# Kernel optimization log

Measured on AMD Instinct MI355X. Metric: run time of the kernel, lower is better.

The kernel has to match this reference:

```python
import jax, jax.numpy as jnp
import numpy as np

N_NODES = 30000
N_EDGES = 480000
N_REL = 16
DIM = 128
N_TRIPLES = 200000


def _xavier(key, shape):
    fan_in, fan_out = shape[-2], shape[-1]
    limit = np.sqrt(6.0 / (fan_in + fan_out)).astype(np.float32)
    return jax.random.uniform(key, shape, jnp.float32, -limit, limit)


def setup_inputs() -> dict:
    key = jax.random.key(0)
    ks = jax.random.split(key, 12)
    inp = {
        "node_emb": _xavier(ks[0], (N_NODES, DIM)),
        "rel_emb": _xavier(ks[1], (N_REL, DIM)),
        "W_rel0": _xavier(ks[2], (N_REL, DIM, DIM)),
        "Wself_w0": _xavier(ks[3], (DIM, DIM)),
        "Wself_b0": jnp.zeros((DIM,), jnp.float32),
        "W_rel1": _xavier(ks[4], (N_REL, DIM, DIM)),
        "Wself_w1": _xavier(ks[5], (DIM, DIM)),
        "Wself_b1": jnp.zeros((DIM,), jnp.float32),
        "local_nodes": jnp.arange(N_NODES, dtype=jnp.int32),
        "edge_index": jax.random.randint(ks[6], (2, N_EDGES), 0, N_NODES, jnp.int32),
        "edge_type": jax.random.randint(ks[7], (N_EDGES,), 0, N_REL, jnp.int32),
        "h_loc": jax.random.randint(ks[8], (N_TRIPLES,), 0, N_NODES, jnp.int32),
        "r_ids": jax.random.randint(ks[9], (N_TRIPLES,), 0, N_REL, jnp.int32),
        "t_loc": jax.random.randint(ks[10], (N_TRIPLES,), 0, N_NODES, jnp.int32),
    }
    return inp


def _rgcn_layer(x, edge_index, edge_type, W_rel, Ww, Wb):
    # x: [N, in], W_rel: [R, in, out], Ww: [out, in] (torch Linear layout)
    N = x.shape[0]
    out = x @ Ww.T + Wb                                 # self loop [N, out]
    src, dst = edge_index[0], edge_index[1]
    # transform every node under every relation, then gather per edge:
    # math-equivalent to bmm(x[src][:,None,:], W_rel[rel]) in the original,
    # but avoids materializing [E, in, out].
    xt = jnp.einsum('ni,rio->rno', x, W_rel)            # [R, N, out]
    msg = xt[edge_type, src]                            # [E, out]
    agg = jax.ops.segment_sum(msg, dst, num_segments=N)  # [N, out]
    deg = jax.ops.segment_sum(jnp.ones(dst.shape, x.dtype), dst, num_segments=N)
    deg = jnp.maximum(deg, 1.0)[:, None]
    return jax.nn.relu(out + agg / deg)


def reference(node_emb, rel_emb, W_rel0, Wself_w0, Wself_b0,
              W_rel1, Wself_w1, Wself_b1,
              local_nodes, edge_index, edge_type, h_loc, r_ids, t_loc):
    x = node_emb[local_nodes]                           # [N, d]
    x = _rgcn_layer(x, edge_index, edge_type, W_rel0, Wself_w0, Wself_b0)
    x = _rgcn_layer(x, edge_index, edge_type, W_rel1, Wself_w1, Wself_b1)
    # DistMult scoring on local embeddings
    scores = jnp.sum(x[h_loc] * rel_emb[r_ids] * x[t_loc], axis=-1)  # [B]
    return scores
```

## Files before the change

### kernel.cpp

```cpp
#include <hip/hip_runtime.h>

#define NN 30000
#define NE 480000
#define NR 16
#define D  128
#define NT 200000
#define AST 132
#define NBLK 235
#define NBINS (NBLK * NR)
#define PF 16


__global__ void k_gather_x(const float* __restrict__ node_emb,
                           const int* __restrict__ local_nodes,
                           float* __restrict__ x) {
  int i4 = blockIdx.x * blockDim.x + threadIdx.x;
  if (i4 >= NN * (D / 4)) return;
  int n = i4 >> 5, c = i4 & 31;
  int src = local_nodes[n];
  reinterpret_cast<float4*>(x)[i4] =
      reinterpret_cast<const float4*>(node_emb)[(size_t)src * 32 + c];
}

__global__ void k_hist_bins(const int* __restrict__ ei, const int* __restrict__ et,
                            int* __restrict__ bins) {
  int e = blockIdx.x * blockDim.x + threadIdx.x;
  if (e >= NE) return;
  int d = ei[NE + e], r = et[e];
  atomicAdd(&bins[(d >> 7) * NR + r], 1);
}

__global__ void k_scan_bins(const int* __restrict__ bins, int* __restrict__ off,
                            int* __restrict__ cur) {
  __shared__ int ps[1024];
  const int t = threadIdx.x;
  const int base = t * 4;
  int c[4], s0 = 0;
#pragma unroll
  for (int u = 0; u < 4; ++u) {
    int b = base + u;
    c[u] = (b < NBINS) ? bins[b] : 0;
    s0 += c[u];
  }
  ps[t] = s0;
  __syncthreads();
  for (int dstep = 1; dstep < 1024; dstep <<= 1) {
    int v = (t >= dstep) ? ps[t - dstep] : 0;
    __syncthreads();
    ps[t] += v;
    __syncthreads();
  }
  int ex = ps[t] - s0;
#pragma unroll
  for (int u = 0; u < 4; ++u) {
    int b = base + u;
    if (b <= NBINS) {
      off[b] = ex;
      if (b < NBINS) cur[b] = ex;
    }
    ex += c[u];
  }
}

__global__ void k_fill(const int* __restrict__ ei, const int* __restrict__ et,
                       int* __restrict__ cur, int* __restrict__ srt,
                       float* __restrict__ deg) {
  int e = blockIdx.x * blockDim.x + threadIdx.x;
  if (e >= NE) return;
  int s = ei[e], d = ei[NE + e], r = et[e];
  int p = atomicAdd(&cur[(d >> 7) * NR + r], 1);
  srt[p] = ((d & 127) << 16) | s;
  atomicAdd(&deg[d], 1.0f);
}

__global__ void k_transposeW(const float* __restrict__ W0, const float* __restrict__ W1,
                             float* __restrict__ T0, float* __restrict__ T1) {
  const float* W = blockIdx.x ? W1 : W0;
  float* T = blockIdx.x ? T1 : T0;
  for (int idx = threadIdx.x; idx < D * D; idx += 256) {
    int o = idx >> 7, k = idx & 127;
    T[k * D + o] = W[idx];
  }
}


__device__ __forceinline__ void gemm_tile(const float (*S)[AST],
                                          const float* __restrict__ Wg,
                                          int tx, int ty, float acc[8][4]) {
  const float4* __restrict__ W4 = reinterpret_cast<const float4*>(Wg);
#pragma unroll 8
  for (int k = 0; k < D; k += 4) {
    float4 a[8];
#pragma unroll
    for (int j = 0; j < 8; ++j)
      a[j] = *reinterpret_cast<const float4*>(&S[ty + 16 * j][k]);
    float4 w[4];
#pragma unroll
    for (int kk = 0; kk < 4; ++kk) w[kk] = W4[(k + kk) * 32 + tx];
#pragma unroll
    for (int kk = 0; kk < 4; ++kk) {
#pragma unroll
      for (int j = 0; j < 8; ++j) {
        float av = (kk == 0) ? a[j].x : (kk == 1) ? a[j].y
                 : (kk == 2) ? a[j].z : a[j].w;
        acc[j][0] += av * w[kk].x;
        acc[j][1] += av * w[kk].y;
        acc[j][2] += av * w[kk].z;
        acc[j][3] += av * w[kk].w;
      }
    }
  }
}

__launch_bounds__(512, 2)
__global__ void k_fused(const float* __restrict__ x, const float* __restrict__ Wrel,
                        const float* __restrict__ WT, const float* __restrict__ Wb,
                        const int* __restrict__ srt, const int* __restrict__ off,
                        const float* __restrict__ deg, float* __restrict__ xo) {
  __shared__ float S[D][AST];
  const int nb = blockIdx.x;
  const int row0 = nb * D;
  const int tx = threadIdx.x & 31, ty = threadIdx.x >> 5;
  const int wave = threadIdx.x >> 6, lane = threadIdx.x & 63;
  const float2* __restrict__ x2 = reinterpret_cast<const float2*>(x);

  float acc[8][4];
#pragma unroll
  for (int j = 0; j < 8; ++j)
#pragma unroll
    for (int m = 0; m < 4; ++m) acc[j][m] = 0.f;

  int pv[PF];
  float2 pvv[PF];

  auto zeroS = [&]() {
    float4* S4 = reinterpret_cast<float4*>(&S[0][0]);
#pragma unroll
    for (int t = 0; t < 9; ++t) {
      int idx = threadIdx.x + 512 * t;
      if (idx < D * AST / 4) S4[idx] = make_float4(0.f, 0.f, 0.f, 0.f);
    }
  };
  auto loadE = [&](int b) {
    const int base = off[b], end = off[b + 1];
#pragma unroll
    for (int t = 0; t < PF; ++t) {
      int i = base + wave + 8 * t;
      pv[t] = (i < end) ? srt[i] : -1;
    }
#pragma unroll
    for (int t = 0; t < PF; ++t)
      pvv[t] = (pv[t] >= 0) ? x2[(size_t)(pv[t] & 0xFFFF) * 64 + lane]
                            : make_float2(0.f, 0.f);
  };
  auto depositE = [&](int b) {
#pragma unroll
    for (int t = 0; t < PF; ++t)
      if (pv[t] >= 0) {
        int dl = pv[t] >> 16;
        atomicAdd(&S[dl][2 * lane], pvv[t].x);
        atomicAdd(&S[dl][2 * lane + 1], pvv[t].y);
      }
    const int end = off[b + 1];
    for (int i = off[b] + 8 * PF + wave; i < end; i += 8) {
      int p = srt[i];
      float2 vv = x2[(size_t)(p & 0xFFFF) * 64 + lane];
      atomicAdd(&S[p >> 16][2 * lane], vv.x);
      atomicAdd(&S[p >> 16][2 * lane + 1], vv.y);
    }
  };

  zeroS();
  __syncthreads();
  loadE(nb * NR);
  depositE(nb * NR);

  for (int r = 0; r < NR; ++r) {
    __syncthreads();
    if (r + 1 < NR) loadE(nb * NR + r + 1);
    gemm_tile(S, Wrel + (size_t)r * D * D, tx, ty, acc);
    __syncthreads();
    zeroS();
    __syncthreads();
    if (r + 1 < NR) depositE(nb * NR + r + 1);
  }

#pragma unroll
  for (int j = 0; j < 8; ++j) {
    int row = row0 + ty + 16 * j;
    float dv = (row < NN) ? deg[row] : 1.f;
    float inv = 1.f / fmaxf(dv, 1.f);
#pragma unroll
    for (int m = 0; m < 4; ++m) acc[j][m] *= inv;
  }

#pragma unroll
  for (int t = 0; t < 8; ++t) {
    int idx = threadIdx.x + 512 * t;
    int rw = idx >> 5, c = idx & 31;
    float4 vv = make_float4(0.f, 0.f, 0.f, 0.f);
    if (row0 + rw < NN)
      vv = reinterpret_cast<const float4*>(x)[(size_t)(row0 + rw) * 32 + c];
    *reinterpret_cast<float4*>(&S[rw][4 * c]) = vv;
  }
  __syncthreads();
  gemm_tile(S, WT, tx, ty, acc);

  const float4 bb = reinterpret_cast<const float4*>(Wb)[tx];
#pragma unroll
  for (int j = 0; j < 8; ++j) {
    int row = row0 + ty + 16 * j;
    if (row < NN) {
      float4 o;
      o.x = fmaxf(acc[j][0] + bb.x, 0.f);
      o.y = fmaxf(acc[j][1] + bb.y, 0.f);
      o.z = fmaxf(acc[j][2] + bb.z, 0.f);
      o.w = fmaxf(acc[j][3] + bb.w, 0.f);
      reinterpret_cast<float4*>(xo + (size_t)row * D)[tx] = o;
    }
  }
}


__global__ void k_score(const float* __restrict__ x, const float* __restrict__ rel,
                        const int* __restrict__ hh, const int* __restrict__ rr,
                        const int* __restrict__ tt, float* __restrict__ out) {
  int gw = (blockIdx.x * blockDim.x + threadIdx.x) >> 6;
  int lane = threadIdx.x & 63;
  int nw = (gridDim.x * blockDim.x) >> 6;
  for (int i = gw; i < NT; i += nw) {
    const float2* ph = reinterpret_cast<const float2*>(x + (size_t)hh[i] * D);
    const float2* pr = reinterpret_cast<const float2*>(rel + (size_t)rr[i] * D);
    const float2* pt = reinterpret_cast<const float2*>(x + (size_t)tt[i] * D);
    float2 a = ph[lane], b = pr[lane], c = pt[lane];
    float v = a.x * b.x * c.x + a.y * b.y * c.y;
#pragma unroll
    for (int m = 32; m; m >>= 1) v += __shfl_xor(v, m);
    if (lane == 0) out[i] = v;
  }
}


extern "C" void kernel_launch(void* const* d_in, const int* in_sizes, int n_in,
                              void* d_out, int out_size, void* d_ws, size_t ws_size,
                              hipStream_t stream) {
  const float* node_emb = (const float*)d_in[0];
  const float* rel_emb  = (const float*)d_in[1];
  const float* W_rel0   = (const float*)d_in[2];
  const float* Wself_w0 = (const float*)d_in[3];
  const float* Wself_b0 = (const float*)d_in[4];
  const float* W_rel1   = (const float*)d_in[5];
  const float* Wself_w1 = (const float*)d_in[6];
  const float* Wself_b1 = (const float*)d_in[7];
  const int* local_nodes = (const int*)d_in[8];
  const int* edge_index  = (const int*)d_in[9];
  const int* edge_type   = (const int*)d_in[10];
  const int* h_loc = (const int*)d_in[11];
  const int* r_ids = (const int*)d_in[12];
  const int* t_loc = (const int*)d_in[13];
  float* out = (float*)d_out;

  char* ws = (char*)d_ws;
  float* x_a = (float*)(ws + 0);
  float* x_b = (float*)(ws + 15360000);
  float* WT0 = (float*)(ws + 30720000);
  float* WT1 = (float*)(ws + 30785536);
  float* deg = (float*)(ws + 30851072);
  int* bins  = (int*)(ws + 30971072);
  int* off   = (int*)(ws + 30986112);
  int* cur   = (int*)(ws + 31001156);
  int* srt   = (int*)(ws + 31016196);
  if (ws_size < (size_t)32936196) return;

  hipMemsetAsync(ws + 30851072, 0, 135040, stream);

  k_gather_x<<<3750, 256, 0, stream>>>(node_emb, local_nodes, x_a);
  k_hist_bins<<<1875, 256, 0, stream>>>(edge_index, edge_type, bins);
  k_scan_bins<<<1, 1024, 0, stream>>>(bins, off, cur);
  k_fill<<<1875, 256, 0, stream>>>(edge_index, edge_type, cur, srt, deg);
  k_transposeW<<<2, 256, 0, stream>>>(Wself_w0, Wself_w1, WT0, WT1);

  k_fused<<<NBLK, 512, 0, stream>>>(x_a, W_rel0, WT0, Wself_b0, srt, off, deg, x_b);
  k_fused<<<NBLK, 512, 0, stream>>>(x_b, W_rel1, WT1, Wself_b1, srt, off, deg, x_a);

  k_score<<<1024, 256, 0, stream>>>(x_a, rel_emb, h_loc, r_ids, t_loc, out);
}
```

Before: 1.479 ms.

## Halve fused RGCN tile rows and double-buffer the aggregation tile

Tiles shrink from 128 to 64 destination rows per block, giving 469 blocks of 256 threads instead of 235 blocks of 512, so the 256 CUs get more even coverage. The shared aggregation tile is now double-buffered: edges for the next relation are scattered into the other buffer while the GEMM for the current one runs, and one barrier per relation is removed. The unpadded S layout may add LDS bank conflicts, and W_rel is now reloaded by twice as many blocks.

Measured after the change: 1.417 ms. 4.2% less time.

```diff
diff --git a/kernel.cpp b/kernel.cpp
--- a/kernel.cpp
+++ b/kernel.cpp
@@ -5,10 +5,10 @@
 #define NR 16
 #define D  128
 #define NT 200000
-#define AST 132
-#define NBLK 235
+#define BR 64
+#define NBLK 469
 #define NBINS (NBLK * NR)
-#define PF 16
+#define PF 24
 
 
 __global__ void k_gather_x(const float* __restrict__ node_emb,
@@ -27,17 +27,17 @@
   int e = blockIdx.x * blockDim.x + threadIdx.x;
   if (e >= NE) return;
   int d = ei[NE + e], r = et[e];
-  atomicAdd(&bins[(d >> 7) * NR + r], 1);
+  atomicAdd(&bins[(d >> 6) * NR + r], 1);
 }
 
 __global__ void k_scan_bins(const int* __restrict__ bins, int* __restrict__ off,
                             int* __restrict__ cur) {
   __shared__ int ps[1024];
   const int t = threadIdx.x;
-  const int base = t * 4;
-  int c[4], s0 = 0;
-#pragma unroll
-  for (int u = 0; u < 4; ++u) {
+  const int base = t * 8;
+  int c[8], s0 = 0;
+#pragma unroll
+  for (int u = 0; u < 8; ++u) {
     int b = base + u;
     c[u] = (b < NBINS) ? bins[b] : 0;
     s0 += c[u];
@@ -52,7 +52,7 @@
   }
   int ex = ps[t] - s0;
 #pragma unroll
-  for (int u = 0; u < 4; ++u) {
+  for (int u = 0; u < 8; ++u) {
     int b = base + u;
     if (b <= NBINS) {
       off[b] = ex;
@@ -68,8 +68,8 @@
   int e = blockIdx.x * blockDim.x + threadIdx.x;
   if (e >= NE) return;
   int s = ei[e], d = ei[NE + e], r = et[e];
-  int p = atomicAdd(&cur[(d >> 7) * NR + r], 1);
-  srt[p] = ((d & 127) << 16) | s;
+  int p = atomicAdd(&cur[(d >> 6) * NR + r], 1);
+  srt[p] = ((d & 63) << 16) | s;
   atomicAdd(&deg[d], 1.0f);
 }
 
@@ -84,7 +84,7 @@
 }
 
 
-__device__ __forceinline__ void gemm_tile(const float (*S)[AST],
+__device__ __forceinline__ void gemm_tile(const float (*S)[D],
                                           const float* __restrict__ Wg,
                                           int tx, int ty, float acc[8][4]) {
   const float4* __restrict__ W4 = reinterpret_cast<const float4*>(Wg);
@@ -93,7 +93,7 @@
     float4 a[8];
 #pragma unroll
     for (int j = 0; j < 8; ++j)
-      a[j] = *reinterpret_cast<const float4*>(&S[ty + 16 * j][k]);
+      a[j] = *reinterpret_cast<const float4*>(&S[ty + 8 * j][k]);
     float4 w[4];
 #pragma unroll
     for (int kk = 0; kk < 4; ++kk) w[kk] = W4[(k + kk) * 32 + tx];
@@ -112,14 +112,14 @@
   }
 }
 
-__launch_bounds__(512, 2)
+__launch_bounds__(256, 2)
 __global__ void k_fused(const float* __restrict__ x, const float* __restrict__ Wrel,
                         const float* __restrict__ WT, const float* __restrict__ Wb,
                         const int* __restrict__ srt, const int* __restrict__ off,
                         const float* __restrict__ deg, float* __restrict__ xo) {
-  __shared__ float S[D][AST];
+  __shared__ float S[2][BR][D];
   const int nb = blockIdx.x;
-  const int row0 = nb * D;
+  const int row0 = nb * BR;
   const int tx = threadIdx.x & 31, ty = threadIdx.x >> 5;
   const int wave = threadIdx.x >> 6, lane = threadIdx.x & 63;
   const float2* __restrict__ x2 = reinterpret_cast<const float2*>(x);
@@ -133,19 +133,17 @@
   int pv[PF];
   float2 pvv[PF];
 
-  auto zeroS = [&]() {
-    float4* S4 = reinterpret_cast<float4*>(&S[0][0]);
-#pragma unroll
-    for (int t = 0; t < 9; ++t) {
-      int idx = threadIdx.x + 512 * t;
-      if (idx < D * AST / 4) S4[idx] = make_float4(0.f, 0.f, 0.f, 0.f);
-    }
+  auto zeroS = [&](int c) {
+    float4* S4 = reinterpret_cast<float4*>(&S[c][0][0]);
+#pragma unroll
+    for (int t = 0; t < 8; ++t)
+      S4[threadIdx.x + 256 * t] = make_float4(0.f, 0.f, 0.f, 0.f);
   };
   auto loadE = [&](int b) {
     const int base = off[b], end = off[b + 1];
 #pragma unroll
     for (int t = 0; t < PF; ++t) {
-      int i = base + wave + 8 * t;
+      int i = base + wave + 4 * t;
       pv[t] = (i < end) ? srt[i] : -1;
     }
 #pragma unroll
@@ -153,41 +151,43 @@
       pvv[t] = (pv[t] >= 0) ? x2[(size_t)(pv[t] & 0xFFFF) * 64 + lane]
                             : make_float2(0.f, 0.f);
   };
-  auto depositE = [&](int b) {
+  auto depositE = [&](int b, int c) {
 #pragma unroll
     for (int t = 0; t < PF; ++t)
       if (pv[t] >= 0) {
         int dl = pv[t] >> 16;
-        atomicAdd(&S[dl][2 * lane], pvv[t].x);
-        atomicAdd(&S[dl][2 * lane + 1], pvv[t].y);
+        atomicAdd(&S[c][dl][2 * lane], pvv[t].x);
+        atomicAdd(&S[c][dl][2 * lane + 1], pvv[t].y);
       }
     const int end = off[b + 1];
-    for (int i = off[b] + 8 * PF + wave; i < end; i += 8) {
+    for (int i = off[b] + 4 * PF + wave; i < end; i += 4) {
       int p = srt[i];
       float2 vv = x2[(size_t)(p & 0xFFFF) * 64 + lane];
-      atomicAdd(&S[p >> 16][2 * lane], vv.x);
-      atomicAdd(&S[p >> 16][2 * lane + 1], vv.y);
+      atomicAdd(&S[c][p >> 16][2 * lane], vv.x);
+      atomicAdd(&S[c][p >> 16][2 * lane + 1], vv.y);
     }
   };
 
-  zeroS();
+  zeroS(0);
+  zeroS(1);
   __syncthreads();
   loadE(nb * NR);
-  depositE(nb * NR);
-
+  depositE(nb * NR, 0);
+
+  int cur = 0;
   for (int r = 0; r < NR; ++r) {
     __syncthreads();
     if (r + 1 < NR) loadE(nb * NR + r + 1);
-    gemm_tile(S, Wrel + (size_t)r * D * D, tx, ty, acc);
-    __syncthreads();
-    zeroS();
-    __syncthreads();
-    if (r + 1 < NR) depositE(nb * NR + r + 1);
+    gemm_tile(S[cur], Wrel + (size_t)r * D * D, tx, ty, acc);
+    if (r + 1 < NR) depositE(nb * NR + r + 1, cur ^ 1);
+    __syncthreads();
+    if (r + 2 < NR) zeroS(cur);
+    cur ^= 1;
   }
 
 #pragma unroll
   for (int j = 0; j < 8; ++j) {
-    int row = row0 + ty + 16 * j;
+    int row = row0 + ty + 8 * j;
     float dv = (row < NN) ? deg[row] : 1.f;
     float inv = 1.f / fmaxf(dv, 1.f);
 #pragma unroll
@@ -196,20 +196,20 @@
 
 #pragma unroll
   for (int t = 0; t < 8; ++t) {
-    int idx = threadIdx.x + 512 * t;
+    int idx = threadIdx.x + 256 * t;
     int rw = idx >> 5, c = idx & 31;
     float4 vv = make_float4(0.f, 0.f, 0.f, 0.f);
     if (row0 + rw < NN)
       vv = reinterpret_cast<const float4*>(x)[(size_t)(row0 + rw) * 32 + c];
-    *reinterpret_cast<float4*>(&S[rw][4 * c]) = vv;
+    *reinterpret_cast<float4*>(&S[0][rw][4 * c]) = vv;
   }
   __syncthreads();
-  gemm_tile(S, WT, tx, ty, acc);
+  gemm_tile(S[0], WT, tx, ty, acc);
 
   const float4 bb = reinterpret_cast<const float4*>(Wb)[tx];
 #pragma unroll
   for (int j = 0; j < 8; ++j) {
-    int row = row0 + ty + 16 * j;
+    int row = row0 + ty + 8 * j;
     if (row < NN) {
       float4 o;
       o.x = fmaxf(acc[j][0] + bb.x, 0.f);
@@ -267,12 +267,12 @@
   float* WT1 = (float*)(ws + 30785536);
   float* deg = (float*)(ws + 30851072);
   int* bins  = (int*)(ws + 30971072);
-  int* off   = (int*)(ws + 30986112);
-  int* cur   = (int*)(ws + 31001156);
-  int* srt   = (int*)(ws + 31016196);
-  if (ws_size < (size_t)32936196) return;
-
-  hipMemsetAsync(ws + 30851072, 0, 135040, stream);
+  int* off   = (int*)(ws + 31001088);
+  int* cur   = (int*)(ws + 31031108);
+  int* srt   = (int*)(ws + 31061124);
+  if (ws_size < (size_t)32981124) return;
+
+  hipMemsetAsync(ws + 30851072, 0, 150016, stream);
 
   k_gather_x<<<3750, 256, 0, stream>>>(node_emb, local_nodes, x_a);
   k_hist_bins<<<1875, 256, 0, stream>>>(edge_index, edge_type, bins);
@@ -280,8 +280,8 @@
   k_fill<<<1875, 256, 0, stream>>>(edge_index, edge_type, cur, srt, deg);
   k_transposeW<<<2, 256, 0, stream>>>(Wself_w0, Wself_w1, WT0, WT1);
 
-  k_fused<<<NBLK, 512, 0, stream>>>(x_a, W_rel0, WT0, Wself_b0, srt, off, deg, x_b);
-  k_fused<<<NBLK, 512, 0, stream>>>(x_b, W_rel1, WT1, Wself_b1, srt, off, deg, x_a);
+  k_fused<<<NBLK, 256, 0, stream>>>(x_a, W_rel0, WT0, Wself_b0, srt, off, deg, x_b);
+  k_fused<<<NBLK, 256, 0, stream>>>(x_b, W_rel1, WT1, Wself_b1, srt, off, deg, x_a);
 
   k_score<<<1024, 256, 0, stream>>>(x_a, rel_emb, h_loc, r_ids, t_loc, out);
 }
```
